# Performance work log

Hardware: AMD Instinct MI355X
Metric: run time of the kernel (lower is better)

The kernel has to match this reference:

```python
import jax, jax.numpy as jnp
import numpy as np

N_NODES = 1048576
N_EDGES = 4 * N_NODES

def _mlp(h, w1, b1, w2, b2):
    return jax.nn.relu(h @ w1 + b1) @ w2 + b2

def setup_inputs() -> dict:
    key = jax.random.key(0)
    ks = jax.random.split(key, 12)
    def glorot(k, shape):
        fan_in, fan_out = shape
        lim = np.sqrt(6.0 / (fan_in + fan_out)).astype(np.float32)
        return jax.random.uniform(k, shape, jnp.float32, -lim, lim)
    x = jax.random.normal(ks[0], (N_NODES, 3), jnp.float32)
    edge_index = jax.random.randint(ks[1], (2, N_EDGES), 0, N_NODES, jnp.int64 if jax.config.jax_enable_x64 else jnp.int32)
    edge_attr = jax.random.normal(ks[2], (N_EDGES, 1), jnp.float32)
    u = jax.random.normal(ks[3], (1, 3), jnp.float32)
    batch = jnp.zeros((N_NODES,), jnp.int32)
    return {
        'x': x, 'edge_index': edge_index, 'edge_attr': edge_attr, 'u': u, 'batch': batch,
        'w1a': glorot(ks[4], (4, 20)), 'b1a': jnp.zeros((20,), jnp.float32),
        'w1b': glorot(ks[5], (20, 3)), 'b1b': jnp.zeros((3,), jnp.float32),
        'w2a': glorot(ks[6], (6, 20)), 'b2a': jnp.zeros((20,), jnp.float32),
        'w2b': glorot(ks[7], (20, 3)), 'b2b': jnp.zeros((3,), jnp.float32),
    }

def reference(x, edge_index, edge_attr, u, batch, w1a, b1a, w1b, b1b, w2a, b2a, w2b, b2b):
    row, col = edge_index[0], edge_index[1]
    n = x.shape[0]
    # gather source node feats, concat edge attr -> [E,4]
    h = jnp.concatenate([x[row], edge_attr], axis=1)
    h = _mlp(h, w1a, b1a, w1b, b1b)                    # [E,3]
    # scatter-mean over destination nodes
    s = jax.ops.segment_sum(h, col, num_segments=n)    # [N,3]
    cnt = jax.ops.segment_sum(jnp.ones((h.shape[0],), h.dtype), col, num_segments=n)
    agg = s / jnp.maximum(cnt, 1.0)[:, None]
    out = _mlp(jnp.concatenate([x, agg], axis=1), w2a, b2a, w2b, b2b)  # [N,3]
    fac = jnp.sqrt(jnp.sum(out ** 2, axis=1, keepdims=True))
    return out / fac
```

## Files before the change

kernel.cpp:

```cpp
#include <hip/hip_runtime.h>


#define SEG  4096
#define P1T  256
#define P1I  (SEG / P1T)
#define BKSH 12
#define BKN  4096
#define NBK  256
#define PFXW 257
#define P2T  1024

union HCvt { _Float16 h; unsigned short u; };

__device__ __forceinline__ float h2f(unsigned short u) {
    HCvt c; c.u = u; return (float)c.h;
}

__device__ __forceinline__ void mlp1_eval(
    float in0, float in1, float in2, float in3,
    const float* sw1a, const float* sb1a, const float* sw1b, const float* sb1b,
    float& o0, float& o1, float& o2)
{
    float h1[20];
#pragma unroll
    for (int j = 0; j < 20; ++j) {
        float v = sb1a[j];
        v = fmaf(in0, sw1a[0 * 20 + j], v);
        v = fmaf(in1, sw1a[1 * 20 + j], v);
        v = fmaf(in2, sw1a[2 * 20 + j], v);
        v = fmaf(in3, sw1a[3 * 20 + j], v);
        h1[j] = v > 0.f ? v : 0.f;
    }
    o0 = sb1b[0]; o1 = sb1b[1]; o2 = sb1b[2];
#pragma unroll
    for (int j = 0; j < 20; ++j) {
        o0 = fmaf(h1[j], sw1b[j * 3 + 0], o0);
        o1 = fmaf(h1[j], sw1b[j * 3 + 1], o1);
        o2 = fmaf(h1[j], sw1b[j * 3 + 2], o2);
    }
    o0 = fminf(fmaxf(o0, -8.0f), 8.0f - 2.0f / 2048.0f);
    o1 = fminf(fmaxf(o1, -8.0f), 8.0f - 2.0f / 2048.0f);
    o2 = fminf(fmaxf(o2, -8.0f), 8.0f - 2.0f / 1024.0f);
}

__device__ __forceinline__ unsigned long long rec_pack(
    unsigned int col_lo, float o0, float o1, float o2)
{
    const unsigned long long q0 = (unsigned int)__float2int_rn((o0 + 8.0f) * 2048.0f);
    const unsigned long long q1 = (unsigned int)__float2int_rn((o1 + 8.0f) * 2048.0f);
    const unsigned long long q2 = (unsigned int)__float2int_rn((o2 + 8.0f) * 1024.0f);
    return (unsigned long long)col_lo | (q0 << 12) | (q1 << 27) | (q2 << 42);
}

__device__ __forceinline__ unsigned long long acc_pack(float o0, float o1, float o2)
{
    const unsigned long long q0 = (unsigned int)__float2int_rn((o0 + 8.0f) * 2048.0f);
    const unsigned long long q1 = (unsigned int)__float2int_rn((o1 + 8.0f) * 2048.0f);
    const unsigned long long q2 = (unsigned int)__float2int_rn((o2 + 8.0f) * 1024.0f);
    return 1ULL | (q0 << 5) | (q1 << 25) | (q2 << 45);
}

__device__ __forceinline__ void mlp2_store(
    unsigned long long q, const float* __restrict__ x, float* __restrict__ out,
    int n, const float* sw2a, const float* sb2a, const float* sw2b, const float* sb2b)
{
    const float cnt = (float)(unsigned int)(q & 31ULL);
    const float f0 = (float)(unsigned int)((q >> 5)  & 0xFFFFFULL);
    const float f1 = (float)(unsigned int)((q >> 25) & 0xFFFFFULL);
    const float f2 = (float)(unsigned int)(q >> 45);
    const float s0 = f0 * (1.0f / 2048.0f) - 8.0f * cnt;
    const float s1 = f1 * (1.0f / 2048.0f) - 8.0f * cnt;
    const float s2 = f2 * (1.0f / 1024.0f) - 8.0f * cnt;
    const float invc = 1.0f / fmaxf(cnt, 1.0f);

    const float in0 = x[n * 3 + 0];
    const float in1 = x[n * 3 + 1];
    const float in2 = x[n * 3 + 2];
    const float in3 = s0 * invc;
    const float in4 = s1 * invc;
    const float in5 = s2 * invc;

    float h1[20];
#pragma unroll
    for (int j = 0; j < 20; ++j) {
        float v = sb2a[j];
        v = fmaf(in0, sw2a[0 * 20 + j], v);
        v = fmaf(in1, sw2a[1 * 20 + j], v);
        v = fmaf(in2, sw2a[2 * 20 + j], v);
        v = fmaf(in3, sw2a[3 * 20 + j], v);
        v = fmaf(in4, sw2a[4 * 20 + j], v);
        v = fmaf(in5, sw2a[5 * 20 + j], v);
        h1[j] = v > 0.f ? v : 0.f;
    }
    float o0 = sb2b[0], o1 = sb2b[1], o2 = sb2b[2];
#pragma unroll
    for (int j = 0; j < 20; ++j) {
        o0 = fmaf(h1[j], sw2b[j * 3 + 0], o0);
        o1 = fmaf(h1[j], sw2b[j * 3 + 1], o1);
        o2 = fmaf(h1[j], sw2b[j * 3 + 2], o2);
    }
    const float inv = 1.0f / sqrtf(o0 * o0 + o1 * o1 + o2 * o2);
    out[n * 3 + 0] = o0 * inv;
    out[n * 3 + 1] = o1 * inv;
    out[n * 3 + 2] = o2 * inv;
}

__global__ __launch_bounds__(256) void pack_x_kernel(
    const float* __restrict__ x, ushort4* __restrict__ xp, int N)
{
    const int n = blockIdx.x * 256 + threadIdx.x;
    if (n >= N) return;
    HCvt c0, c1, c2;
    c0.h = (_Float16)x[n * 3 + 0];
    c1.h = (_Float16)x[n * 3 + 1];
    c2.h = (_Float16)x[n * 3 + 2];
    ushort4 r; r.x = c0.u; r.y = c1.u; r.z = c2.u; r.w = 0;
    xp[n] = r;
}

__global__ __launch_bounds__(P1T) void p1_kernel(
    const ushort4* __restrict__ xp,
    const int*   __restrict__ edge_index,
    const float* __restrict__ edge_attr,
    const float* __restrict__ w1a, const float* __restrict__ b1a,
    const float* __restrict__ w1b, const float* __restrict__ b1b,
    unsigned short* __restrict__ pfx_tr,
    unsigned long long* __restrict__ vals,
    int E, int nsegs)
{
    __shared__ float sw1a[80], sb1a[20], sw1b[60], sb1b[3];
    __shared__ unsigned int hist[NBK];
    __shared__ unsigned int sc[NBK];
    __shared__ unsigned int pfx[PFXW];
    __shared__ __align__(16) unsigned long long svals[SEG];
    const int t = threadIdx.x;
    if (t < 80) sw1a[t] = w1a[t];
    if (t < 20) sb1a[t] = b1a[t];
    if (t < 60) sw1b[t] = w1b[t];
    if (t < 3)  sb1b[t] = b1b[t];
    hist[t] = 0;
    __syncthreads();

    const int s = blockIdx.x;
    const int base = s * SEG;

    unsigned int col8[P1I];
#pragma unroll
    for (int i = 0; i < P1I; ++i) {
        const int e = base + i * P1T + t;
        if (e < E) {
            const unsigned int c = (unsigned int)edge_index[E + e];
            col8[i] = c;
            atomicAdd(&hist[c >> BKSH], 1u);
        } else {
            col8[i] = 0xFFFFFFFFu;
        }
    }
    __syncthreads();

    sc[t] = hist[t];
    __syncthreads();
#pragma unroll
    for (int off = 1; off < NBK; off <<= 1) {
        const unsigned int u = (t >= off) ? sc[t - off] : 0u;
        __syncthreads();
        sc[t] += u;
        __syncthreads();
    }
    pfx[t + 1] = sc[t];
    if (t == 0) pfx[0] = 0;
    hist[t] = 0;
    __syncthreads();

    pfx_tr[(size_t)t * nsegs + s] = (unsigned short)pfx[t];
    if (t == 0) pfx_tr[(size_t)NBK * nsegs + s] = (unsigned short)pfx[NBK];

#pragma unroll
    for (int i = 0; i < P1I; ++i) {
        const unsigned int c = col8[i];
        if (c == 0xFFFFFFFFu) continue;
        const int e = base + i * P1T + t;
        const int row = edge_index[e];
        const float in3 = edge_attr[e];
        const ushort4 px = xp[row];
        float o0, o1, o2;
        mlp1_eval(h2f(px.x), h2f(px.y), h2f(px.z), in3,
                  sw1a, sb1a, sw1b, sb1b, o0, o1, o2);
        const unsigned int bkt = c >> BKSH;
        const unsigned int r = atomicAdd(&hist[bkt], 1u);
        const unsigned int idx = pfx[bkt] + r;
        svals[idx] = rec_pack(c & (BKN - 1), o0, o1, o2);
    }
    __syncthreads();

    unsigned long long* gv = vals + (size_t)base;
#pragma unroll
    for (int k = t; k < SEG; k += P1T) gv[k] = svals[k];
}

__global__ __launch_bounds__(P2T) void p2_kernel(
    const float* __restrict__ x,
    const unsigned short* __restrict__ pfx_tr,
    const unsigned long long* __restrict__ vals,
    const float* __restrict__ w2a, const float* __restrict__ b2a,
    const float* __restrict__ w2b, const float* __restrict__ b2b,
    float* __restrict__ out,
    int N, int nsegs)
{
    __shared__ float sw2a[120], sb2a[20], sw2b[60], sb2b[3];
    __shared__ unsigned long long acc[BKN];
    const int t = threadIdx.x;
    if (t < 120) sw2a[t] = w2a[t];
    if (t < 20)  sb2a[t] = b2a[t];
    if (t < 60)  sw2b[t] = w2b[t];
    if (t < 3)   sb2b[t] = b2b[t];
#pragma unroll
    for (int k = 0; k < BKN / P2T; ++k) acc[k * P2T + t] = 0ULL;
    __syncthreads();

    const int b = blockIdx.x;
    const int wave = t >> 6;
    const int lane = t & 63;
    const unsigned short* rowa = pfx_tr + (size_t)b * nsegs;
    const unsigned short* rowb = pfx_tr + (size_t)(b + 1) * nsegs;

    for (int s = wave; s < nsegs; s += P2T / 64) {
        const unsigned int pa = rowa[s];
        const unsigned int pb = rowb[s];
        const size_t base = (size_t)s * SEG;
        for (unsigned int i = pa + lane; i < pb; i += 64) {
            const unsigned long long rec = vals[base + i];
            const unsigned int c = (unsigned int)(rec & 0xFFFULL);
            const unsigned long long q0 = (rec >> 12) & 0x7FFFULL;
            const unsigned long long q1 = (rec >> 27) & 0x7FFFULL;
            const unsigned long long q2 = (rec >> 42) & 0x3FFFULL;
            const unsigned long long add =
                1ULL | (q0 << 5) | (q1 << 25) | (q2 << 45);
            atomicAdd(&acc[c], add);
        }
    }
    __syncthreads();

    const int node0 = b * BKN;
#pragma unroll
    for (int k = 0; k < BKN / P2T; ++k) {
        const int n = node0 + k * P2T + t;
        if (n >= N) continue;
        mlp2_store(acc[k * P2T + t], x, out, n, sw2a, sb2a, sw2b, sb2b);
    }
}

__global__ __launch_bounds__(256) void edge_kernel_fb(
    const float* __restrict__ x, const int* __restrict__ edge_index,
    const float* __restrict__ edge_attr,
    const float* __restrict__ w1a, const float* __restrict__ b1a,
    const float* __restrict__ w1b, const float* __restrict__ b1b,
    unsigned long long* __restrict__ acc, int E)
{
    __shared__ float sw1a[80], sb1a[20], sw1b[60], sb1b[3];
    const int t = threadIdx.x;
    if (t < 80) sw1a[t] = w1a[t];
    if (t < 20) sb1a[t] = b1a[t];
    if (t < 60) sw1b[t] = w1b[t];
    if (t < 3)  sb1b[t] = b1b[t];
    __syncthreads();
    const int e = blockIdx.x * 256 + t;
    if (e >= E) return;
    const int row = edge_index[e];
    const int col = edge_index[E + e];
    float o0, o1, o2;
    mlp1_eval(x[row * 3 + 0], x[row * 3 + 1], x[row * 3 + 2], edge_attr[e],
              sw1a, sb1a, sw1b, sb1b, o0, o1, o2);
    atomicAdd(acc + col, acc_pack(o0, o1, o2));
}

__global__ __launch_bounds__(256) void node_kernel_fb(
    const float* __restrict__ x, const unsigned long long* __restrict__ acc,
    const float* __restrict__ w2a, const float* __restrict__ b2a,
    const float* __restrict__ w2b, const float* __restrict__ b2b,
    float* __restrict__ out, int N)
{
    __shared__ float sw2a[120], sb2a[20], sw2b[60], sb2b[3];
    const int t = threadIdx.x;
    if (t < 120) sw2a[t] = w2a[t];
    if (t < 20)  sb2a[t] = b2a[t];
    if (t < 60)  sw2b[t] = w2b[t];
    if (t < 3)   sb2b[t] = b2b[t];
    __syncthreads();
    const int n = blockIdx.x * 256 + t;
    if (n >= N) return;
    mlp2_store(acc[n], x, out, n, sw2a, sb2a, sw2b, sb2b);
}

extern "C" void kernel_launch(void* const* d_in, const int* in_sizes, int n_in,
                              void* d_out, int out_size, void* d_ws, size_t ws_size,
                              hipStream_t stream) {
    const float* x          = (const float*)d_in[0];
    const int*   edge_index = (const int*)  d_in[1];
    const float* edge_attr  = (const float*)d_in[2];
    const float* w1a = (const float*)d_in[5];
    const float* b1a = (const float*)d_in[6];
    const float* w1b = (const float*)d_in[7];
    const float* b1b = (const float*)d_in[8];
    const float* w2a = (const float*)d_in[9];
    const float* b2a = (const float*)d_in[10];
    const float* w2b = (const float*)d_in[11];
    const float* b2b = (const float*)d_in[12];

    const int N = in_sizes[0] / 3;
    const int E = in_sizes[2];

    const int nbuckets = (N + BKN - 1) / BKN;
    const int nsegs = (E + SEG - 1) / SEG;

    const size_t xp_bytes  = (size_t)N * sizeof(ushort4);
    const size_t pfx_off   = (xp_bytes + 255) & ~(size_t)255;
    const size_t pfx_bytes = (size_t)PFXW * nsegs * sizeof(unsigned short);
    const size_t vals_off  = (pfx_off + pfx_bytes + 255) & ~(size_t)255;
    const size_t need      = vals_off + (size_t)nsegs * SEG * sizeof(unsigned long long);

    const bool fast = (nbuckets <= NBK) && (ws_size >= need);

    if (fast) {
        ushort4* xp = (ushort4*)d_ws;
        unsigned short* pfx_tr = (unsigned short*)((char*)d_ws + pfx_off);
        unsigned long long* vals = (unsigned long long*)((char*)d_ws + vals_off);

        pack_x_kernel<<<(N + 255) / 256, 256, 0, stream>>>(x, xp, N);

        p1_kernel<<<nsegs, P1T, 0, stream>>>(
            xp, edge_index, edge_attr, w1a, b1a, w1b, b1b,
            pfx_tr, vals, E, nsegs);

        p2_kernel<<<nbuckets, P2T, 0, stream>>>(
            x, pfx_tr, vals, w2a, b2a, w2b, b2b, (float*)d_out, N, nsegs);
    } else {
        unsigned long long* acc = (unsigned long long*)d_ws;
        hipMemsetAsync(acc, 0, (size_t)N * sizeof(unsigned long long), stream);
        edge_kernel_fb<<<(E + 255) / 256, 256, 0, stream>>>(
            x, edge_index, edge_attr, w1a, b1a, w1b, b1b, acc, E);
        node_kernel_fb<<<(N + 255) / 256, 256, 0, stream>>>(
            x, acc, w2a, b2a, w2b, b2b, (float*)d_out, N);
    }
}
```

Baseline: 240.4 us.

## Split edge MLP from bucket sort and assign 16 lanes per segment in aggregation

The fused edge pass becomes two kernels. The first evaluates the edge MLP per edge with light shared memory, so more waves can be resident and hide the random gathers of xp. The second runs the bucket histogram and scatter in place on the record buffer using the stored payloads. The aggregation kernel now splits each wave into four 16-lane groups, each handling a different segment, because each segment-bucket run is short and a full 64-lane wave left most lanes idle. The cost is an extra launch and an extra global round trip of 8 bytes per edge.

```diff
diff --git a/kernel.cpp b/kernel.cpp
--- a/kernel.cpp
+++ b/kernel.cpp
@@ -2,8 +2,8 @@
 
 
 #define SEG  4096
-#define P1T  256
-#define P1I  (SEG / P1T)
+#define P1BT 256
+#define P1BI (SEG / P1BT)
 #define BKSH 12
 #define BKN  4096
 #define NBK  256
@@ -43,13 +43,12 @@
     o2 = fminf(fmaxf(o2, -8.0f), 8.0f - 2.0f / 1024.0f);
 }
 
-__device__ __forceinline__ unsigned long long rec_pack(
-    unsigned int col_lo, float o0, float o1, float o2)
+__device__ __forceinline__ unsigned long long payload_pack(float o0, float o1, float o2)
 {
     const unsigned long long q0 = (unsigned int)__float2int_rn((o0 + 8.0f) * 2048.0f);
     const unsigned long long q1 = (unsigned int)__float2int_rn((o1 + 8.0f) * 2048.0f);
     const unsigned long long q2 = (unsigned int)__float2int_rn((o2 + 8.0f) * 1024.0f);
-    return (unsigned long long)col_lo | (q0 << 12) | (q1 << 27) | (q2 << 42);
+    return (q0 << 12) | (q1 << 27) | (q2 << 42);
 }
 
 __device__ __forceinline__ unsigned long long acc_pack(float o0, float o1, float o2)
@@ -118,36 +117,56 @@
     xp[n] = r;
 }
 
-__global__ __launch_bounds__(P1T) void p1_kernel(
+__global__ __launch_bounds__(256) void p1a_kernel(
     const ushort4* __restrict__ xp,
     const int*   __restrict__ edge_index,
     const float* __restrict__ edge_attr,
     const float* __restrict__ w1a, const float* __restrict__ b1a,
     const float* __restrict__ w1b, const float* __restrict__ b1b,
+    unsigned long long* __restrict__ recs,
+    int E)
+{
+    __shared__ float sw1a[80], sb1a[20], sw1b[60], sb1b[3];
+    const int t = threadIdx.x;
+    if (t < 80) sw1a[t] = w1a[t];
+    if (t < 20) sb1a[t] = b1a[t];
+    if (t < 60) sw1b[t] = w1b[t];
+    if (t < 3)  sb1b[t] = b1b[t];
+    __syncthreads();
+
+    const int e = blockIdx.x * 256 + t;
+    if (e >= E) return;
+
+    const int row = edge_index[e];
+    const float attr = edge_attr[e];
+    const ushort4 px = xp[row];
+    float o0, o1, o2;
+    mlp1_eval(h2f(px.x), h2f(px.y), h2f(px.z), attr,
+              sw1a, sb1a, sw1b, sb1b, o0, o1, o2);
+    recs[e] = payload_pack(o0, o1, o2);
+}
+
+__global__ __launch_bounds__(P1BT) void p1b_kernel(
+    const int* __restrict__ edge_index,
+    unsigned long long* __restrict__ recs,
     unsigned short* __restrict__ pfx_tr,
-    unsigned long long* __restrict__ vals,
     int E, int nsegs)
 {
-    __shared__ float sw1a[80], sb1a[20], sw1b[60], sb1b[3];
     __shared__ unsigned int hist[NBK];
     __shared__ unsigned int sc[NBK];
     __shared__ unsigned int pfx[PFXW];
     __shared__ __align__(16) unsigned long long svals[SEG];
     const int t = threadIdx.x;
-    if (t < 80) sw1a[t] = w1a[t];
-    if (t < 20) sb1a[t] = b1a[t];
-    if (t < 60) sw1b[t] = w1b[t];
-    if (t < 3)  sb1b[t] = b1b[t];
     hist[t] = 0;
     __syncthreads();
 
     const int s = blockIdx.x;
     const int base = s * SEG;
 
-    unsigned int col8[P1I];
-#pragma unroll
-    for (int i = 0; i < P1I; ++i) {
-        const int e = base + i * P1T + t;
+    unsigned int col8[P1BI];
+#pragma unroll
+    for (int i = 0; i < P1BI; ++i) {
+        const int e = base + i * P1BT + t;
         if (e < E) {
             const unsigned int c = (unsigned int)edge_index[E + e];
             col8[i] = c;
@@ -176,26 +195,21 @@
     if (t == 0) pfx_tr[(size_t)NBK * nsegs + s] = (unsigned short)pfx[NBK];
 
 #pragma unroll
-    for (int i = 0; i < P1I; ++i) {
+    for (int i = 0; i < P1BI; ++i) {
         const unsigned int c = col8[i];
         if (c == 0xFFFFFFFFu) continue;
-        const int e = base + i * P1T + t;
-        const int row = edge_index[e];
-        const float in3 = edge_attr[e];
-        const ushort4 px = xp[row];
-        float o0, o1, o2;
-        mlp1_eval(h2f(px.x), h2f(px.y), h2f(px.z), in3,
-                  sw1a, sb1a, sw1b, sb1b, o0, o1, o2);
+        const int e = base + i * P1BT + t;
+        const unsigned long long rec =
+            recs[e] | (unsigned long long)(c & (BKN - 1));
         const unsigned int bkt = c >> BKSH;
         const unsigned int r = atomicAdd(&hist[bkt], 1u);
-        const unsigned int idx = pfx[bkt] + r;
-        svals[idx] = rec_pack(c & (BKN - 1), o0, o1, o2);
-    }
-    __syncthreads();
-
-    unsigned long long* gv = vals + (size_t)base;
-#pragma unroll
-    for (int k = t; k < SEG; k += P1T) gv[k] = svals[k];
+        svals[pfx[bkt] + r] = rec;
+    }
+    __syncthreads();
+
+    unsigned long long* gv = recs + (size_t)base;
+#pragma unroll
+    for (int k = t; k < SEG; k += P1BT) gv[k] = svals[k];
 }
 
 __global__ __launch_bounds__(P2T) void p2_kernel(
@@ -221,22 +235,27 @@
     const int b = blockIdx.x;
     const int wave = t >> 6;
     const int lane = t & 63;
+    const int sub  = lane >> 4;
+    const int sl   = lane & 15;
     const unsigned short* rowa = pfx_tr + (size_t)b * nsegs;
     const unsigned short* rowb = pfx_tr + (size_t)(b + 1) * nsegs;
 
-    for (int s = wave; s < nsegs; s += P2T / 64) {
-        const unsigned int pa = rowa[s];
-        const unsigned int pb = rowb[s];
-        const size_t base = (size_t)s * SEG;
-        for (unsigned int i = pa + lane; i < pb; i += 64) {
-            const unsigned long long rec = vals[base + i];
-            const unsigned int c = (unsigned int)(rec & 0xFFFULL);
-            const unsigned long long q0 = (rec >> 12) & 0x7FFFULL;
-            const unsigned long long q1 = (rec >> 27) & 0x7FFFULL;
-            const unsigned long long q2 = (rec >> 42) & 0x3FFFULL;
-            const unsigned long long add =
-                1ULL | (q0 << 5) | (q1 << 25) | (q2 << 45);
-            atomicAdd(&acc[c], add);
+    for (int sg = wave * 4; sg < nsegs; sg += (P2T / 64) * 4) {
+        const int s = sg + sub;
+        if (s < nsegs) {
+            const unsigned int pa = rowa[s];
+            const unsigned int pb = rowb[s];
+            const size_t base = (size_t)s * SEG;
+            for (unsigned int i = pa + sl; i < pb; i += 16) {
+                const unsigned long long rec = vals[base + i];
+                const unsigned int c = (unsigned int)(rec & 0xFFFULL);
+                const unsigned long long q0 = (rec >> 12) & 0x7FFFULL;
+                const unsigned long long q1 = (rec >> 27) & 0x7FFFULL;
+                const unsigned long long q2 = (rec >> 42) & 0x3FFFULL;
+                const unsigned long long add =
+                    1ULL | (q0 << 5) | (q1 << 25) | (q2 << 45);
+                atomicAdd(&acc[c], add);
+            }
         }
     }
     __syncthreads();
@@ -313,27 +332,29 @@
     const int nbuckets = (N + BKN - 1) / BKN;
     const int nsegs = (E + SEG - 1) / SEG;
 
-    const size_t xp_bytes  = (size_t)N * sizeof(ushort4);
-    const size_t pfx_off   = (xp_bytes + 255) & ~(size_t)255;
-    const size_t pfx_bytes = (size_t)PFXW * nsegs * sizeof(unsigned short);
-    const size_t vals_off  = (pfx_off + pfx_bytes + 255) & ~(size_t)255;
-    const size_t need      = vals_off + (size_t)nsegs * SEG * sizeof(unsigned long long);
+    const size_t xp_bytes   = (size_t)N * sizeof(ushort4);
+    const size_t recs_off   = (xp_bytes + 255) & ~(size_t)255;
+    const size_t recs_bytes = (size_t)nsegs * SEG * sizeof(unsigned long long);
+    const size_t pfx_off    = (recs_off + recs_bytes + 255) & ~(size_t)255;
+    const size_t need       = pfx_off + (size_t)PFXW * nsegs * sizeof(unsigned short);
 
     const bool fast = (nbuckets <= NBK) && (ws_size >= need);
 
     if (fast) {
         ushort4* xp = (ushort4*)d_ws;
+        unsigned long long* recs = (unsigned long long*)((char*)d_ws + recs_off);
         unsigned short* pfx_tr = (unsigned short*)((char*)d_ws + pfx_off);
-        unsigned long long* vals = (unsigned long long*)((char*)d_ws + vals_off);
 
         pack_x_kernel<<<(N + 255) / 256, 256, 0, stream>>>(x, xp, N);
 
-        p1_kernel<<<nsegs, P1T, 0, stream>>>(
-            xp, edge_index, edge_attr, w1a, b1a, w1b, b1b,
-            pfx_tr, vals, E, nsegs);
+        p1a_kernel<<<(E + 255) / 256, 256, 0, stream>>>(
+            xp, edge_index, edge_attr, w1a, b1a, w1b, b1b, recs, E);
+
+        p1b_kernel<<<nsegs, P1BT, 0, stream>>>(
+            edge_index, recs, pfx_tr, E, nsegs);
 
         p2_kernel<<<nbuckets, P2T, 0, stream>>>(
-            x, pfx_tr, vals, w2a, b2a, w2b, b2b, (float*)d_out, N, nsegs);
+            x, pfx_tr, recs, w2a, b2a, w2b, b2b, (float*)d_out, N, nsegs);
     } else {
         unsigned long long* acc = (unsigned long long*)d_ws;
         hipMemsetAsync(acc, 0, (size_t)N * sizeof(unsigned long long), stream);
```

Result: faster. 222.6 us (-7.4%).
